# Performance work log

Hardware: AMD Instinct MI355X
Metric: run time of the kernel (lower is better)

Reference implementation:

```python
import jax, jax.numpy as jnp
import numpy as np

POOL_H, POOL_W = 7, 7


def crop_and_resize(fmap, boxes, box_idx, ph, pw):
    """TF-style bilinear crop_and_resize. fmap [B,H,W,C], boxes [N,4] (y1,x1,y2,x2)
    normalized, box_idx [N] int32 -> [N,ph,pw,C]."""
    H, W = fmap.shape[1], fmap.shape[2]
    y1, x1, y2, x2 = boxes[:, 0], boxes[:, 1], boxes[:, 2], boxes[:, 3]
    gy = jnp.arange(ph, dtype=boxes.dtype) / (ph - 1)  # [ph]
    gx = jnp.arange(pw, dtype=boxes.dtype) / (pw - 1)  # [pw]
    in_y = (y1[:, None] + (y2 - y1)[:, None] * gy) * (H - 1)  # [N,ph]
    in_x = (x1[:, None] + (x2 - x1)[:, None] * gx) * (W - 1)  # [N,pw]
    y0f = jnp.floor(in_y)
    x0f = jnp.floor(in_x)
    wy = (in_y - y0f)[:, :, None, None]  # [N,ph,1,1]
    wx = (in_x - x0f)[:, None, :, None]  # [N,1,pw,1]
    y0 = jnp.clip(y0f.astype(jnp.int32), 0, H - 1)
    y1i = jnp.clip(y0 + 1, 0, H - 1)
    x0 = jnp.clip(x0f.astype(jnp.int32), 0, W - 1)
    x1i = jnp.clip(x0 + 1, 0, W - 1)
    b = box_idx[:, None, None]
    tl = fmap[b, y0[:, :, None], x0[:, None, :]]   # [N,ph,pw,C]
    tr = fmap[b, y0[:, :, None], x1i[:, None, :]]
    bl = fmap[b, y1i[:, :, None], x0[:, None, :]]
    br = fmap[b, y1i[:, :, None], x1i[:, None, :]]
    top = tl + (tr - tl) * wx
    bot = bl + (br - bl) * wx
    return top + (bot - top) * wy


def compute_roi_level(boxes, image_shape):
    # boxes [B,N,4] normalized (y1,x1,y2,x2)
    h = boxes[..., 2] - boxes[..., 0]
    w = boxes[..., 3] - boxes[..., 1]
    image_area = image_shape[0] * image_shape[1]
    lvl = jnp.log2(jnp.sqrt(h * w) / (224.0 / jnp.sqrt(image_area)))
    lvl = jnp.minimum(5.0, jnp.maximum(2.0, 4.0 + jnp.round(lvl)))
    return jax.lax.stop_gradient(lvl).astype(jnp.int32)  # [B,N]


def setup_inputs() -> dict:
    key = jax.random.key(0)
    kb, k2, k3, k4, k5 = jax.random.split(key, 5)
    B, N, C = 2, 1000, 256
    raw = jax.random.uniform(kb, (B, N, 2, 2), dtype=jnp.float32)
    lo = raw.min(axis=2)   # (y1, x1)
    hi = raw.max(axis=2)   # (y2, x2)
    boxes = jnp.concatenate([lo, hi], axis=-1)  # [B,N,4]
    image_shape = jnp.array([1024.0, 1024.0], dtype=jnp.float32)
    P2 = jax.random.normal(k2, (B, 256, 256, C), dtype=jnp.float32)
    P3 = jax.random.normal(k3, (B, 128, 128, C), dtype=jnp.float32)
    P4 = jax.random.normal(k4, (B, 64, 64, C), dtype=jnp.float32)
    P5 = jax.random.normal(k5, (B, 32, 32, C), dtype=jnp.float32)
    return {"boxes": boxes, "image_shape": image_shape,
            "P2": P2, "P3": P3, "P4": P4, "P5": P5}


def reference(boxes, image_shape, P2, P3, P4, P5):
    B, N = boxes.shape[0], boxes.shape[1]
    C = P2.shape[-1]
    levels = compute_roi_level(boxes, image_shape).reshape(-1)  # [B*N]
    flat_boxes = boxes.reshape(-1, 4)
    box_idx = jnp.repeat(jnp.arange(B, dtype=jnp.int32), N)
    pooled = jnp.zeros((B * N, POOL_H, POOL_W, C), dtype=P2.dtype)
    for lvl, fmap in zip((2, 3, 4, 5), (P2, P3, P4, P5)):
        crops = crop_and_resize(fmap, flat_boxes, box_idx, POOL_H, POOL_W)
        mask = (levels == lvl)[:, None, None, None]
        pooled = jnp.where(mask, crops, pooled)
    # The TF version partitions boxes per level then sorts back to original
    # (batch, box) order; the masked-select form yields the identical tensor.
    return pooled.reshape(B, N, POOL_H, POOL_W, C)
```

## Files before the change

### kernel.cpp

```cpp
#include <hip/hip_runtime.h>


#define POOL 7
#define CCH 256

__global__ __launch_bounds__(256) void roi_align_kernel(
    const float* __restrict__ boxes,
    const float* __restrict__ ish,
    const float* __restrict__ P2,
    const float* __restrict__ P3,
    const float* __restrict__ P4,
    const float* __restrict__ P5,
    float* __restrict__ out,
    int n_cells, int N)
{
    int cell = blockIdx.x * 4 + (threadIdx.x >> 6);
    if (cell >= n_cells) return;
    int lane = threadIdx.x & 63;

    int px  = cell % POOL;
    int t   = cell / POOL;
    int py  = t % POOL;
    int n   = t / POOL;
    int b   = n / N;

    float y1 = boxes[n * 4 + 0];
    float x1 = boxes[n * 4 + 1];
    float y2 = boxes[n * 4 + 2];
    float x2 = boxes[n * 4 + 3];
    float h = y2 - y1;
    float w = x2 - x1;

    float area = ish[0] * ish[1];
    float lvl  = log2f(sqrtf(h * w) / (224.0f / sqrtf(area)));
    float Lf   = fminf(5.0f, fmaxf(2.0f, 4.0f + rintf(lvl)));
    int   L    = (int)Lf;

    const float* fmap;
    int H;
    if (L == 2)      { fmap = P2; H = 256; }
    else if (L == 3) { fmap = P3; H = 128; }
    else if (L == 4) { fmap = P4; H = 64;  }
    else             { fmap = P5; H = 32;  }
    int W = H;

    float gy = (float)py / (float)(POOL - 1);
    float gx = (float)px / (float)(POOL - 1);
    float in_y = (y1 + h * gy) * (float)(H - 1);
    float in_x = (x1 + w * gx) * (float)(W - 1);
    float y0f = floorf(in_y);
    float x0f = floorf(in_x);
    float wy = in_y - y0f;
    float wx = in_x - x0f;
    int y0  = min(max((int)y0f, 0), H - 1);
    int y1i = min(y0 + 1, H - 1);
    int x0  = min(max((int)x0f, 0), W - 1);
    int x1i = min(x0 + 1, W - 1);

    size_t base = (size_t)b * H * W * CCH;
    const float* ptl = fmap + base + ((size_t)y0  * W + x0 ) * CCH;
    const float* ptr = fmap + base + ((size_t)y0  * W + x1i) * CCH;
    const float* pbl = fmap + base + ((size_t)y1i * W + x0 ) * CCH;
    const float* pbr = fmap + base + ((size_t)y1i * W + x1i) * CCH;

    int c = lane * 4;
    float4 tl = *(const float4*)(ptl + c);
    float4 tr = *(const float4*)(ptr + c);
    float4 bl = *(const float4*)(pbl + c);
    float4 br = *(const float4*)(pbr + c);

    float4 o;
    {
        float top, bot;
        top = tl.x + (tr.x - tl.x) * wx;
        bot = bl.x + (br.x - bl.x) * wx;
        o.x = top + (bot - top) * wy;
        top = tl.y + (tr.y - tl.y) * wx;
        bot = bl.y + (br.y - bl.y) * wx;
        o.y = top + (bot - top) * wy;
        top = tl.z + (tr.z - tl.z) * wx;
        bot = bl.z + (br.z - bl.z) * wx;
        o.z = top + (bot - top) * wy;
        top = tl.w + (tr.w - tl.w) * wx;
        bot = bl.w + (br.w - bl.w) * wx;
        o.w = top + (bot - top) * wy;
    }

    *(float4*)(out + (size_t)cell * CCH + c) = o;
}

extern "C" void kernel_launch(void* const* d_in, const int* in_sizes, int n_in,
                              void* d_out, int out_size, void* d_ws, size_t ws_size,
                              hipStream_t stream)
{
    const float* boxes = (const float*)d_in[0];
    const float* ish   = (const float*)d_in[1];
    const float* P2    = (const float*)d_in[2];
    const float* P3    = (const float*)d_in[3];
    const float* P4    = (const float*)d_in[4];
    const float* P5    = (const float*)d_in[5];
    float* out = (float*)d_out;

    int total_boxes = in_sizes[0] / 4;
    int B = in_sizes[2] / (256 * 256 * CCH);
    int N = total_boxes / B;
    int n_cells = total_boxes * POOL * POOL;

    int blocks = (n_cells + 3) / 4;
    roi_align_kernel<<<blocks, 256, 0, stream>>>(boxes, ish, P2, P3, P4, P5,
                                                 out, n_cells, N);
}
```

Before: 250.1 us.

## Process one pooled row per wavefront with unrolled loop and nontemporal stores

Each wavefront now handles a whole output row of 7 cells instead of a single cell. The box load, level selection and y interpolation are computed once per row rather than per cell, and the seven cells' loads are unrolled so more memory requests are in flight at once. Output writes use nontemporal stores so the write stream does not pollute the cache. The grid shrinks sevenfold (14000 rows / 4 = 3500 blocks), which lowers parallelism and raises per-thread register use.

```diff
diff --git a/kernel.cpp b/kernel.cpp
--- a/kernel.cpp
+++ b/kernel.cpp
@@ -4,7 +4,9 @@
 #define POOL 7
 #define CCH 256
 
-__global__ __launch_bounds__(256) void roi_align_kernel(
+typedef float f32x4 __attribute__((ext_vector_type(4)));
+
+__global__ __launch_bounds__(256) void roi_align_row_kernel(
     const float* __restrict__ boxes,
     const float* __restrict__ ish,
     const float* __restrict__ P2,
@@ -12,17 +14,17 @@
     const float* __restrict__ P4,
     const float* __restrict__ P5,
     float* __restrict__ out,
-    int n_cells, int N)
+    int n_rows, int N)
 {
-    int cell = blockIdx.x * 4 + (threadIdx.x >> 6);
-    if (cell >= n_cells) return;
-    int lane = threadIdx.x & 63;
+    int row = blockIdx.x * 4 + (threadIdx.x >> 6);
+    if (row >= n_rows) return;
+    row = __builtin_amdgcn_readfirstlane(row);
+    const int lane = threadIdx.x & 63;
+    const int c = lane * 4;
 
-    int px  = cell % POOL;
-    int t   = cell / POOL;
-    int py  = t % POOL;
-    int n   = t / POOL;
-    int b   = n / N;
+    int py = row % POOL;
+    int n  = row / POOL;
+    int b  = n / N;
 
     float y1 = boxes[n * 4 + 0];
     float x1 = boxes[n * 4 + 1];
@@ -42,51 +44,43 @@
     else if (L == 3) { fmap = P3; H = 128; }
     else if (L == 4) { fmap = P4; H = 64;  }
     else             { fmap = P5; H = 32;  }
-    int W = H;
+    const int W = H;
 
-    float gy = (float)py / (float)(POOL - 1);
-    float gx = (float)px / (float)(POOL - 1);
+    float gy   = (float)py / (float)(POOL - 1);
     float in_y = (y1 + h * gy) * (float)(H - 1);
-    float in_x = (x1 + w * gx) * (float)(W - 1);
-    float y0f = floorf(in_y);
-    float x0f = floorf(in_x);
-    float wy = in_y - y0f;
-    float wx = in_x - x0f;
+    float y0f  = floorf(in_y);
+    float wy   = in_y - y0f;
     int y0  = min(max((int)y0f, 0), H - 1);
     int y1i = min(y0 + 1, H - 1);
-    int x0  = min(max((int)x0f, 0), W - 1);
-    int x1i = min(x0 + 1, W - 1);
 
     size_t base = (size_t)b * H * W * CCH;
-    const float* ptl = fmap + base + ((size_t)y0  * W + x0 ) * CCH;
-    const float* ptr = fmap + base + ((size_t)y0  * W + x1i) * CCH;
-    const float* pbl = fmap + base + ((size_t)y1i * W + x0 ) * CCH;
-    const float* pbr = fmap + base + ((size_t)y1i * W + x1i) * CCH;
+    const float* rowT = fmap + base + (size_t)y0  * W * CCH + c;
+    const float* rowB = fmap + base + (size_t)y1i * W * CCH + c;
 
-    int c = lane * 4;
-    float4 tl = *(const float4*)(ptl + c);
-    float4 tr = *(const float4*)(ptr + c);
-    float4 bl = *(const float4*)(pbl + c);
-    float4 br = *(const float4*)(pbr + c);
+    float* orow = out + (size_t)row * POOL * CCH + c;
 
-    float4 o;
-    {
-        float top, bot;
-        top = tl.x + (tr.x - tl.x) * wx;
-        bot = bl.x + (br.x - bl.x) * wx;
-        o.x = top + (bot - top) * wy;
-        top = tl.y + (tr.y - tl.y) * wx;
-        bot = bl.y + (br.y - bl.y) * wx;
-        o.y = top + (bot - top) * wy;
-        top = tl.z + (tr.z - tl.z) * wx;
-        bot = bl.z + (br.z - bl.z) * wx;
-        o.z = top + (bot - top) * wy;
-        top = tl.w + (tr.w - tl.w) * wx;
-        bot = bl.w + (br.w - bl.w) * wx;
-        o.w = top + (bot - top) * wy;
+    #pragma unroll
+    for (int px = 0; px < POOL; ++px) {
+        float gx   = (float)px / (float)(POOL - 1);
+        float in_x = (x1 + w * gx) * (float)(W - 1);
+        float x0f  = floorf(in_x);
+        float wx   = in_x - x0f;
+        int x0  = min(max((int)x0f, 0), W - 1);
+        int x1i = min(x0 + 1, W - 1);
+        int o0 = x0  * CCH;
+        int o1 = x1i * CCH;
+
+        f32x4 tl = *(const f32x4*)(rowT + o0);
+        f32x4 tr = *(const f32x4*)(rowT + o1);
+        f32x4 bl = *(const f32x4*)(rowB + o0);
+        f32x4 br = *(const f32x4*)(rowB + o1);
+
+        f32x4 top = tl + (tr - tl) * wx;
+        f32x4 bot = bl + (br - bl) * wx;
+        f32x4 o   = top + (bot - top) * wy;
+
+        __builtin_nontemporal_store(o, (f32x4*)(orow + px * CCH));
     }
-
-    *(float4*)(out + (size_t)cell * CCH + c) = o;
 }
 
 extern "C" void kernel_launch(void* const* d_in, const int* in_sizes, int n_in,
@@ -104,9 +98,9 @@
     int total_boxes = in_sizes[0] / 4;
     int B = in_sizes[2] / (256 * 256 * CCH);
     int N = total_boxes / B;
-    int n_cells = total_boxes * POOL * POOL;
+    int n_rows = total_boxes * POOL;
 
-    int blocks = (n_cells + 3) / 4;
-    roi_align_kernel<<<blocks, 256, 0, stream>>>(boxes, ish, P2, P3, P4, P5,
-                                                 out, n_cells, N);
+    int blocks = (n_rows + 3) / 4;
+    roi_align_row_kernel<<<blocks, 256, 0, stream>>>(boxes, ish, P2, P3, P4, P5,
+                                                     out, n_rows, N);
 }
```

Result: no change. 252.8 us (+1.1%).
